# Kernel optimization log

Hardware: AMD Instinct MI355X
Metric: run time of the kernel (lower is better)

The kernel has to match this reference:

```python
import jax, jax.numpy as jnp
import numpy as np

BATCH, E = 4096, 8
DIMS = [512, 1024, 1024, 512]


def setup_inputs() -> dict:
    key = jax.random.key(0)
    ks = jax.random.split(key, 8)
    inp = {
        'weight_blend': jax.random.uniform(ks[0], (BATCH, E), dtype=jnp.float32),
        'x': jax.random.normal(ks[1], (BATCH, DIMS[0]), dtype=jnp.float32),
    }
    for i in range(3):
        inp[f'W{i}'] = jax.random.normal(ks[2 + i], (E, DIMS[i + 1], DIMS[i]), dtype=jnp.float32)
        inp[f'B{i}'] = jnp.zeros((E, DIMS[i + 1]), dtype=jnp.float32)
    return inp


def _blended_layer(weight_blend, x, W, B):
    # Fused form of: weight = sum_e blend[b,e]*W[e]; y = bmm(weight, x) + sum_e blend[b,e]*B[e]
    # Computed as sum_e blend_e * (W_e @ x) without materializing (batch,out,in).
    y = jnp.einsum('eoi,bi->beo', W, x)          # per-expert GEMM, (B,E,out)
    y = jnp.einsum('be,beo->bo', weight_blend, y)  # blend combine
    return y + weight_blend @ B                   # blended bias (B,out)


def reference(weight_blend, x, W0, B0, W1, B1, W2, B2):
    # Dropout with keep_prob=0.0 is identity in eval mode; activations: elu, elu, linear.
    h = jax.nn.elu(_blended_layer(weight_blend, x, W0, B0))
    h = jax.nn.elu(_blended_layer(weight_blend, h, W1, B1))
    out = _blended_layer(weight_blend, h, W2, B2)
    return out
```

## Files before the change

kernel.cpp:

```cpp
#include <hip/hip_runtime.h>
#include <cstdint>
#include <cstddef>

typedef __bf16 bf16x8 __attribute__((ext_vector_type(8)));
typedef float f32x4 __attribute__((ext_vector_type(4)));
typedef unsigned short u16;
typedef unsigned short u16x8 __attribute__((ext_vector_type(8)));

#define BATCH 4096
#define NE 8

__device__ __forceinline__ u16 f2bf(float f) {
  union { float f; uint32_t u; } v; v.f = f;
  uint32_t u = v.u;
  u += 0x7fffu + ((u >> 16) & 1u);
  return (u16)(u >> 16);
}

__device__ __forceinline__ float bf2f(u16 u) {
  union { uint32_t u; float f; } v; v.u = ((uint32_t)u) << 16;
  return v.f;
}

__device__ __forceinline__ void cast8(const float* src, u16* dst) {
  const float4* p = (const float4*)src;
  float4 a = p[0], b = p[1];
  u16x8 o;
  o[0] = f2bf(a.x); o[1] = f2bf(a.y); o[2] = f2bf(a.z); o[3] = f2bf(a.w);
  o[4] = f2bf(b.x); o[5] = f2bf(b.y); o[6] = f2bf(b.z); o[7] = f2bf(b.w);
  *(u16x8*)dst = o;
}

__device__ __forceinline__ void conv_w_chunk(const float* __restrict__ W,
                                             u16* __restrict__ Bt,
                                             int N, int K0, int chunk) {
  int per_row = K0 >> 3;
  int rid = chunk / per_row;
  int i0 = (chunk - rid * per_row) << 3;
  int e = rid / N;
  int o = rid - e * N;
  cast8(W + (size_t)rid * K0 + i0,
        Bt + (size_t)o * ((size_t)NE * K0) + (size_t)e * K0 + i0);
}

__global__ void prep_kernel(const float* __restrict__ x,
                            const float* __restrict__ W0,
                            const float* __restrict__ W1,
                            const float* __restrict__ W2,
                            u16* __restrict__ h0, u16* __restrict__ Bt0,
                            u16* __restrict__ Bt1, u16* __restrict__ Bt2) {
  int t = blockIdx.x * blockDim.x + threadIdx.x;
  const int C0 = BATCH * 512 / 8;
  const int C1 = C0 + NE * 1024 * 512 / 8;
  const int C2 = C1 + NE * 1024 * 1024 / 8;
  if (t < C0) {
    cast8(x + (size_t)t * 8, h0 + (size_t)t * 8);
  } else if (t < C1) {
    conv_w_chunk(W0, Bt0, 1024, 512, t - C0);
  } else if (t < C2) {
    conv_w_chunk(W1, Bt1, 1024, 1024, t - C1);
  } else {
    conv_w_chunk(W2, Bt2, 512, 1024, t - C2);
  }
}

template<bool ELU_ACT, bool OUT_BF16>
__global__ void combine8_kernel(const u16* __restrict__ P,
                                const float* __restrict__ blend,
                                const float* __restrict__ Bias,
                                void* __restrict__ outp, int N) {
  int t = blockIdx.x * blockDim.x + threadIdx.x;
  int per_row = N >> 3;
  int b = t / per_row;
  int i0 = (t - b * per_row) << 3;
  const size_t slice = (size_t)BATCH * N;
  const float4* blp = (const float4*)(blend + b * NE);
  float4 u0 = blp[0], u1 = blp[1];
  float bl[8] = {u0.x, u0.y, u0.z, u0.w, u1.x, u1.y, u1.z, u1.w};
  float v[8] = {0, 0, 0, 0, 0, 0, 0, 0};
  #pragma unroll
  for (int e = 0; e < NE; ++e) {
    u16x8 pv = *(const u16x8*)(P + (size_t)e * slice + (size_t)b * N + i0);
    #pragma unroll
    for (int j = 0; j < 8; ++j) v[j] += bl[e] * bf2f(pv[j]);
  }
  #pragma unroll
  for (int e = 0; e < NE; ++e) {
    const float4* bp = (const float4*)(Bias + (size_t)e * N + i0);
    float4 ba = bp[0], bb = bp[1];
    float bv[8] = {ba.x, ba.y, ba.z, ba.w, bb.x, bb.y, bb.z, bb.w};
    #pragma unroll
    for (int j = 0; j < 8; ++j) v[j] += bl[e] * bv[j];
  }
  if (ELU_ACT) {
    #pragma unroll
    for (int j = 0; j < 8; ++j) v[j] = v[j] > 0.f ? v[j] : expm1f(v[j]);
  }
  if (OUT_BF16) {
    u16x8 o;
    #pragma unroll
    for (int j = 0; j < 8; ++j) o[j] = f2bf(v[j]);
    *(u16x8*)((u16*)outp + (size_t)b * N + i0) = o;
  } else {
    float4* op = (float4*)((float*)outp + (size_t)b * N + i0);
    op[0] = (float4){v[0], v[1], v[2], v[3]};
    op[1] = (float4){v[4], v[5], v[6], v[7]};
  }
}

#define GL2LDS(g, l) __builtin_amdgcn_global_load_lds( \
    (__attribute__((address_space(1))) void*)(g),      \
    (__attribute__((address_space(3))) void*)(l), 16, 0, 0)

template<int K0>
__global__ __launch_bounds__(256, 4)
void gemm_be_kernel(const u16* __restrict__ h, const u16* __restrict__ Bt,
                    u16* __restrict__ P, int N) {
  __shared__ __align__(16) u16 Hs[128 * 64];
  __shared__ __align__(16) u16 Bs[128 * 64];

  const int tid  = threadIdx.x;
  const int w    = tid >> 6, lane = tid & 63;
  const int wm   = w >> 1,   wn   = w & 1;
  const int lrow = lane & 15, quad = lane >> 4;

  const int row0 = blockIdx.x * 128;
  const int col0 = blockIdx.y * 128;
  const int e    = blockIdx.z;
  const int EK   = K0 * NE;

  const int trow = tid >> 3;
  const int tcol = (tid & 7) ^ (trow & 7);
  const u16* gH = h + (size_t)(row0 + trow) * K0 + (tcol << 3);
  const u16* gB = Bt + (size_t)(col0 + trow) * EK + (size_t)e * K0 + (tcol << 3);
  u16* lH = &Hs[tid * 8];
  u16* lB = &Bs[tid * 8];

  const int xr = lrow & 7;
  const u16* fH[2][4];
  const u16* fB[2][4];
  #pragma unroll
  for (int kc = 0; kc < 2; ++kc)
    #pragma unroll
    for (int i = 0; i < 4; ++i) {
      fH[kc][i] = &Hs[(wm * 64 + i * 16 + lrow) * 64 + (((kc * 4 + quad) ^ xr) << 3)];
      fB[kc][i] = &Bs[(wn * 64 + i * 16 + lrow) * 64 + (((kc * 4 + quad) ^ xr) << 3)];
    }

  f32x4 acc[4][4];
  #pragma unroll
  for (int i = 0; i < 4; ++i)
    #pragma unroll
    for (int j = 0; j < 4; ++j) acc[i][j] = (f32x4){0.f, 0.f, 0.f, 0.f};

  for (int it = 0; it < K0 / 64; ++it) {
    #pragma unroll
    for (int i = 0; i < 4; ++i) {
      GL2LDS(gH + (size_t)(32 * i) * K0, lH + 2048 * i);
      GL2LDS(gB + (size_t)(32 * i) * EK, lB + 2048 * i);
    }
    gH += 64; gB += 64;
    __syncthreads();

    #pragma unroll
    for (int kc = 0; kc < 2; ++kc) {
      bf16x8 hf[4], bfr[4];
      #pragma unroll
      for (int i = 0; i < 4; ++i) hf[i] = *(const bf16x8*)fH[kc][i];
      #pragma unroll
      for (int j = 0; j < 4; ++j) bfr[j] = *(const bf16x8*)fB[kc][j];
      #pragma unroll
      for (int i = 0; i < 4; ++i)
        #pragma unroll
        for (int j = 0; j < 4; ++j)
          acc[i][j] = __builtin_amdgcn_mfma_f32_16x16x32_bf16(hf[i], bfr[j], acc[i][j], 0, 0, 0);
    }
    __syncthreads();
  }

  u16* Ps = P + (size_t)e * ((size_t)BATCH * N);
  #pragma unroll
  for (int mt = 0; mt < 4; ++mt) {
    #pragma unroll
    for (int r = 0; r < 4; ++r) {
      int row = row0 + wm * 64 + mt * 16 + quad * 4 + r;
      #pragma unroll
      for (int nt = 0; nt < 4; ++nt) {
        int col = col0 + wn * 64 + nt * 16 + lrow;
        Ps[(size_t)row * N + col] = f2bf(acc[mt][nt][r]);
      }
    }
  }
}

extern "C" void kernel_launch(void* const* d_in, const int* in_sizes, int n_in,
                              void* d_out, int out_size, void* d_ws, size_t ws_size,
                              hipStream_t stream) {
  const float* blend = (const float*)d_in[0];
  const float* x  = (const float*)d_in[1];
  const float* W0 = (const float*)d_in[2];
  const float* B0 = (const float*)d_in[3];
  const float* W1 = (const float*)d_in[4];
  const float* B1 = (const float*)d_in[5];
  const float* W2 = (const float*)d_in[6];
  const float* B2 = (const float*)d_in[7];
  float* out = (float*)d_out;

  char* ws = (char*)d_ws;
  u16* hA  = (u16*)ws;
  u16* h1  = (u16*)(ws + 8388608);
  u16* Bt0 = (u16*)(ws + 16777216);
  u16* Bt1 = (u16*)(ws + 25165824);
  u16* Bt2 = (u16*)(ws + 41943040);
  u16* P   = (u16*)(ws + 50331648);

  prep_kernel<<<9216, 256, 0, stream>>>(x, W0, W1, W2, hA, Bt0, Bt1, Bt2);

  gemm_be_kernel<512><<<dim3(32, 8, 8), 256, 0, stream>>>(hA, Bt0, P, 1024);
  combine8_kernel<true, true><<<2048, 256, 0, stream>>>(P, blend, B0, h1, 1024);

  gemm_be_kernel<1024><<<dim3(32, 8, 8), 256, 0, stream>>>(h1, Bt1, P, 1024);
  combine8_kernel<true, true><<<2048, 256, 0, stream>>>(P, blend, B1, hA, 1024);

  gemm_be_kernel<1024><<<dim3(32, 4, 8), 256, 0, stream>>>(hA, Bt2, P, 512);
  combine8_kernel<false, false><<<1024, 256, 0, stream>>>(P, blend, B2, out, 512);
}
```

Measured before the change: 330.7 us.

## Load B fragments directly from global and stage epilogue stores through LDS

The GEMM no longer stages the weight tile in shared memory. Each wave loads its B operand fragments straight from global memory into registers, and only the activation tile goes through LDS. The epilogue now writes accumulators into a swizzled LDS buffer per wave and then emits 16-byte coalesced stores instead of scattered 2-byte stores. Launch bounds drop to 3 blocks per CU to leave room for the extra registers. This halves LDS traffic and shared memory use, but the B reads are now uncached, per-wave global loads that other waves re-read redundantly, and occupancy is lower.

```diff
diff --git a/kernel.cpp b/kernel.cpp
--- a/kernel.cpp
+++ b/kernel.cpp
@@ -113,11 +113,10 @@
     (__attribute__((address_space(3))) void*)(l), 16, 0, 0)
 
 template<int K0>
-__global__ __launch_bounds__(256, 4)
+__global__ __launch_bounds__(256, 3)
 void gemm_be_kernel(const u16* __restrict__ h, const u16* __restrict__ Bt,
                     u16* __restrict__ P, int N) {
   __shared__ __align__(16) u16 Hs[128 * 64];
-  __shared__ __align__(16) u16 Bs[128 * 64];
 
   const int tid  = threadIdx.x;
   const int w    = tid >> 6, lane = tid & 63;
@@ -132,20 +131,23 @@
   const int trow = tid >> 3;
   const int tcol = (tid & 7) ^ (trow & 7);
   const u16* gH = h + (size_t)(row0 + trow) * K0 + (tcol << 3);
-  const u16* gB = Bt + (size_t)(col0 + trow) * EK + (size_t)e * K0 + (tcol << 3);
   u16* lH = &Hs[tid * 8];
-  u16* lB = &Bs[tid * 8];
 
   const int xr = lrow & 7;
   const u16* fH[2][4];
-  const u16* fB[2][4];
   #pragma unroll
   for (int kc = 0; kc < 2; ++kc)
     #pragma unroll
-    for (int i = 0; i < 4; ++i) {
+    for (int i = 0; i < 4; ++i)
       fH[kc][i] = &Hs[(wm * 64 + i * 16 + lrow) * 64 + (((kc * 4 + quad) ^ xr) << 3)];
-      fB[kc][i] = &Bs[(wn * 64 + i * 16 + lrow) * 64 + (((kc * 4 + quad) ^ xr) << 3)];
-    }
+
+  const u16* gBf[8];
+  #pragma unroll
+  for (int kc = 0; kc < 2; ++kc)
+    #pragma unroll
+    for (int nt = 0; nt < 4; ++nt)
+      gBf[kc * 4 + nt] = Bt + (size_t)(col0 + wn * 64 + nt * 16 + lrow) * EK
+                            + (size_t)e * K0 + kc * 32 + quad * 8;
 
   f32x4 acc[4][4];
   #pragma unroll
@@ -155,40 +157,55 @@
 
   for (int it = 0; it < K0 / 64; ++it) {
     #pragma unroll
-    for (int i = 0; i < 4; ++i) {
+    for (int i = 0; i < 4; ++i)
       GL2LDS(gH + (size_t)(32 * i) * K0, lH + 2048 * i);
-      GL2LDS(gB + (size_t)(32 * i) * EK, lB + 2048 * i);
-    }
-    gH += 64; gB += 64;
+    gH += 64;
+    bf16x8 bfr[8];
+    #pragma unroll
+    for (int j = 0; j < 8; ++j)
+      bfr[j] = *(const bf16x8*)(gBf[j] + it * 64);
     __syncthreads();
 
     #pragma unroll
     for (int kc = 0; kc < 2; ++kc) {
-      bf16x8 hf[4], bfr[4];
+      bf16x8 hf[4];
       #pragma unroll
       for (int i = 0; i < 4; ++i) hf[i] = *(const bf16x8*)fH[kc][i];
       #pragma unroll
-      for (int j = 0; j < 4; ++j) bfr[j] = *(const bf16x8*)fB[kc][j];
-      #pragma unroll
       for (int i = 0; i < 4; ++i)
         #pragma unroll
-        for (int j = 0; j < 4; ++j)
-          acc[i][j] = __builtin_amdgcn_mfma_f32_16x16x32_bf16(hf[i], bfr[j], acc[i][j], 0, 0, 0);
+        for (int nt = 0; nt < 4; ++nt)
+          acc[i][nt] = __builtin_amdgcn_mfma_f32_16x16x32_bf16(hf[i], bfr[kc * 4 + nt], acc[i][nt], 0, 0, 0);
     }
     __syncthreads();
   }
 
   u16* Ps = P + (size_t)e * ((size_t)BATCH * N);
-  #pragma unroll
-  for (int mt = 0; mt < 4; ++mt) {
-    #pragma unroll
-    for (int r = 0; r < 4; ++r) {
-      int row = row0 + wm * 64 + mt * 16 + quad * 4 + r;
+  u16* ls = &Hs[w * 2048];
+  #pragma unroll
+  for (int half = 0; half < 2; ++half) {
+    #pragma unroll
+    for (int mh = 0; mh < 2; ++mh) {
+      int mt = half * 2 + mh;
       #pragma unroll
-      for (int nt = 0; nt < 4; ++nt) {
-        int col = col0 + wn * 64 + nt * 16 + lrow;
-        Ps[(size_t)row * N + col] = f2bf(acc[mt][nt][r]);
+      for (int r = 0; r < 4; ++r) {
+        int rloc = mh * 16 + quad * 4 + r;
+        #pragma unroll
+        for (int nt = 0; nt < 4; ++nt) {
+          int col = nt * 16 + lrow;
+          int c8 = (col >> 3) ^ (rloc & 7);
+          ls[rloc * 64 + (c8 << 3) + (col & 7)] = f2bf(acc[mt][nt][r]);
+        }
       }
+    }
+    #pragma unroll
+    for (int p = 0; p < 4; ++p) {
+      int rloc = p * 8 + (lane >> 3);
+      int c8 = (lane & 7) ^ (rloc & 7);
+      u16x8 v = *(const u16x8*)&ls[rloc * 64 + (c8 << 3)];
+      int row = row0 + wm * 64 + half * 32 + rloc;
+      int colg = col0 + wn * 64 + ((lane & 7) << 3);
+      *(u16x8*)&Ps[(size_t)row * N + colg] = v;
     }
   }
 }
```

New measurement: 444.3 us. 1.34x slower.

## Stage GEMM epilogue through LDS for vector stores and remap block order

Applied to the files above, without the earlier changes.

The GEMM epilogue now writes accumulators into a swizzled LDS tile per wave and then issues 16-byte vectorized global stores, replacing scattered 2-byte stores. The 3D grid is also flattened so consecutive blocks share the same row tile of activations across experts and column tiles, which is meant to improve L2 reuse of the h operand. The epilogue reuses the Hs buffer after the final sync, which costs extra LDS traffic and sync-free per-wave staging.

```diff
diff --git a/kernel.cpp b/kernel.cpp
--- a/kernel.cpp
+++ b/kernel.cpp
@@ -112,7 +112,7 @@
     (__attribute__((address_space(1))) void*)(g),      \
     (__attribute__((address_space(3))) void*)(l), 16, 0, 0)
 
-template<int K0>
+template<int K0, int NB>
 __global__ __launch_bounds__(256, 4)
 void gemm_be_kernel(const u16* __restrict__ h, const u16* __restrict__ Bt,
                     u16* __restrict__ P, int N) {
@@ -124,9 +124,14 @@
   const int wm   = w >> 1,   wn   = w & 1;
   const int lrow = lane & 15, quad = lane >> 4;
 
-  const int row0 = blockIdx.x * 128;
-  const int col0 = blockIdx.y * 128;
-  const int e    = blockIdx.z;
+  const int bid    = blockIdx.x;
+  const int combos = NB * NE;
+  const int combo  = bid % combos;
+  const int rowb   = bid / combos;
+  const int e      = combo & 7;
+  const int colb   = combo >> 3;
+  const int row0 = rowb * 128;
+  const int col0 = colb * 128;
   const int EK   = K0 * NE;
 
   const int trow = tid >> 3;
@@ -179,16 +184,31 @@
   }
 
   u16* Ps = P + (size_t)e * ((size_t)BATCH * N);
-  #pragma unroll
-  for (int mt = 0; mt < 4; ++mt) {
-    #pragma unroll
-    for (int r = 0; r < 4; ++r) {
-      int row = row0 + wm * 64 + mt * 16 + quad * 4 + r;
-      #pragma unroll
-      for (int nt = 0; nt < 4; ++nt) {
-        int col = col0 + wn * 64 + nt * 16 + lrow;
-        Ps[(size_t)row * N + col] = f2bf(acc[mt][nt][r]);
+  u16* ls = &Hs[w * 2048];
+  #pragma unroll
+  for (int half = 0; half < 2; ++half) {
+    #pragma unroll
+    for (int mh = 0; mh < 2; ++mh) {
+      int mt = half * 2 + mh;
+      #pragma unroll
+      for (int r = 0; r < 4; ++r) {
+        int rloc = mh * 16 + quad * 4 + r;
+        #pragma unroll
+        for (int nt = 0; nt < 4; ++nt) {
+          int col = nt * 16 + lrow;
+          int c8 = (col >> 3) ^ (rloc & 7);
+          ls[rloc * 64 + (c8 << 3) + (col & 7)] = f2bf(acc[mt][nt][r]);
+        }
       }
+    }
+    #pragma unroll
+    for (int p = 0; p < 4; ++p) {
+      int rloc = p * 8 + (lane >> 3);
+      int c8 = (lane & 7) ^ (rloc & 7);
+      u16x8 v = *(const u16x8*)&ls[rloc * 64 + (c8 << 3)];
+      int row = row0 + wm * 64 + half * 32 + rloc;
+      int colg = col0 + wn * 64 + ((lane & 7) << 3);
+      *(u16x8*)&Ps[(size_t)row * N + colg] = v;
     }
   }
 }
@@ -216,12 +236,12 @@
 
   prep_kernel<<<9216, 256, 0, stream>>>(x, W0, W1, W2, hA, Bt0, Bt1, Bt2);
 
-  gemm_be_kernel<512><<<dim3(32, 8, 8), 256, 0, stream>>>(hA, Bt0, P, 1024);
+  gemm_be_kernel<512, 8><<<2048, 256, 0, stream>>>(hA, Bt0, P, 1024);
   combine8_kernel<true, true><<<2048, 256, 0, stream>>>(P, blend, B0, h1, 1024);
 
-  gemm_be_kernel<1024><<<dim3(32, 8, 8), 256, 0, stream>>>(h1, Bt1, P, 1024);
+  gemm_be_kernel<1024, 8><<<2048, 256, 0, stream>>>(h1, Bt1, P, 1024);
   combine8_kernel<true, true><<<2048, 256, 0, stream>>>(P, blend, B1, hA, 1024);
 
-  gemm_be_kernel<1024><<<dim3(32, 4, 8), 256, 0, stream>>>(hA, Bt2, P, 512);
+  gemm_be_kernel<1024, 4><<<1024, 256, 0, stream>>>(hA, Bt2, P, 512);
   combine8_kernel<false, false><<<1024, 256, 0, stream>>>(P, blend, B2, out, 512);
 }
```

New measurement: 347.9 us. 5.2% more time.
